# Kernel tuning notes

Measured on AMD Instinct MI355X. Metric: run time of the kernel, lower is better.

## Reference

```python
import jax, jax.numpy as jnp
import numpy as np

B, T, D, H = 4, 2048, 2048, 16
DH = D // H

def setup_inputs() -> dict:
    key = jax.random.key(0)
    ks = jax.random.split(key, 9)
    s = 1.0 / np.sqrt(D)
    return {
        "x": jax.random.normal(ks[0], (B, T, D), dtype=jnp.float32),
        "Wq": jax.random.uniform(ks[1], (D, D), jnp.float32, -s, s),
        "bq": jax.random.uniform(ks[2], (D,), jnp.float32, -s, s),
        "Wk": jax.random.uniform(ks[3], (D, D), jnp.float32, -s, s),
        "bk": jax.random.uniform(ks[4], (D,), jnp.float32, -s, s),
        "Wv": jax.random.uniform(ks[5], (D, D), jnp.float32, -s, s),
        "bv": jax.random.uniform(ks[6], (D,), jnp.float32, -s, s),
        "Wo": jax.random.uniform(ks[7], (D, D), jnp.float32, -s, s),
        "bo": jax.random.uniform(ks[8], (D,), jnp.float32, -s, s),
    }

def reference(x, Wq, bq, Wk, bk, Wv, bv, Wo, bo):
    # projections: [B,T,D] -> [B,H,T,DH]
    def split_heads(y):
        return y.reshape(B, T, H, DH).transpose(0, 2, 1, 3)
    q = split_heads(x @ Wq + bq)
    k = split_heads(x @ Wk + bk)
    v = split_heads(x @ Wv + bv)
    scale = DH ** -0.5
    scores = jnp.einsum('bhtd,bhsd->bhts', q, k) * scale  # [B,H,T,T]
    causal = jnp.tril(jnp.ones((T, T), dtype=bool))
    scores = jnp.where(causal[None, None], scores, -jnp.inf)
    weights = jax.nn.softmax(scores, axis=-1)
    out = jnp.einsum('bhts,bhsd->bhtd', weights, v)  # [B,H,T,DH]
    out = out.transpose(0, 2, 1, 3).reshape(B, T, D)
    return out @ Wo + bo
```

## Files before the change

### kernel.cpp

```cpp
#include <hip/hip_runtime.h>
#include <hip/hip_bf16.h>

#define B_  4
#define T_  2048
#define D_  2048
#define H_  16
#define DH_ 128

typedef __attribute__((ext_vector_type(4))) float f32x4;
typedef __attribute__((ext_vector_type(8))) short short8;
typedef __attribute__((ext_vector_type(4))) _Float16 half4;

__device__ __forceinline__ ushort f2bf(float f) {
    unsigned int u = __builtin_bit_cast(unsigned int, f);
    u += 0x7fffu + ((u >> 16) & 1u);
    return (ushort)(u >> 16);
}
__device__ __forceinline__ ushort f2h(float f) {
    return (ushort)(__builtin_bit_cast(unsigned int, __builtin_amdgcn_cvt_pkrtz(f, f)) & 0xffffu);
}

__device__ __forceinline__ void glds16(const void* g, void* l) {
    __builtin_amdgcn_global_load_lds(
        (const __attribute__((address_space(1))) unsigned int*)g,
        (__attribute__((address_space(3))) unsigned int*)l, 16, 0, 0);
}

__global__ void cast_f32_bf16(const float* __restrict__ x, ushort* __restrict__ xb, int n) {
    int i = (blockIdx.x * 256 + threadIdx.x) * 4;
    if (i < n) {
        float4 v = *(const float4*)(x + i);
        ushort4 o;
        o.x = f2bf(v.x); o.y = f2bf(v.y); o.z = f2bf(v.z); o.w = f2bf(v.w);
        *(ushort4*)(xb + i) = o;
    }
}

__global__ void transpose_cast(const float* __restrict__ W, ushort* __restrict__ Wt) {
    __shared__ float tile[32][33];
    int tx = threadIdx.x, ty = threadIdx.y;
    int n0 = blockIdx.x * 32, k0 = blockIdx.y * 32;
#pragma unroll
    for (int i = 0; i < 4; i++)
        tile[ty + i * 8][tx] = W[(size_t)(k0 + ty + i * 8) * D_ + n0 + tx];
    __syncthreads();
#pragma unroll
    for (int i = 0; i < 4; i++)
        Wt[(size_t)(n0 + ty + i * 8) * D_ + k0 + tx] = f2bf(tile[tx][ty + i * 8]);
}

template <int MODE>
__global__ __launch_bounds__(256, 2) void gemm_bt(
    const ushort* __restrict__ A, const ushort* __restrict__ Bt,
    const float* __restrict__ bias, void* __restrict__ Cout,
    int M, int N, int K, float oscale)
{
    extern __shared__ char smem[];
    uint4* sA = (uint4*)smem;
    uint4* sB = (uint4*)(smem + 8192);

    const int tid  = threadIdx.x;
    const int row0 = blockIdx.y * 128, col0 = blockIdx.x * 128;

    const int mA = tid >> 2, g = tid & 3;
    const int gc = g ^ ((mA >> 2) & 3);
    const ushort* pa0 = A  + (size_t)(row0 + mA) * K + gc * 8;
    const ushort* pb0 = Bt + (size_t)(col0 + mA) * K + gc * 8;

    const int lane = tid & 63, w = tid >> 6;
    const int l15 = lane & 15, quad = lane >> 4;
    const int wm = w & 1, wn = w >> 1;
    const int csel = quad ^ ((l15 >> 2) & 3);
    int aoff[4], boff[4];
#pragma unroll
    for (int mt = 0; mt < 4; mt++) aoff[mt] = (wm * 64 + mt * 16 + l15) * 4 + csel;
#pragma unroll
    for (int nt = 0; nt < 4; nt++) boff[nt] = (wn * 64 + nt * 16 + l15) * 4 + csel;

    f32x4 acc[4][4] = {};

    const int kIter = K >> 5;
    for (int kt = 0; kt < kIter; ++kt) {
        if (kt) __syncthreads();
        glds16(pa0 + kt * 32,                     sA + tid);
        glds16(pa0 + kt * 32 + (size_t)64 * K,    sA + tid + 256);
        glds16(pb0 + kt * 32,                     sB + tid);
        glds16(pb0 + kt * 32 + (size_t)64 * K,    sB + tid + 256);
        __syncthreads();
        short8 af[4], bfr[4];
#pragma unroll
        for (int mt = 0; mt < 4; mt++) af[mt]  = __builtin_bit_cast(short8, sA[aoff[mt]]);
#pragma unroll
        for (int nt = 0; nt < 4; nt++) bfr[nt] = __builtin_bit_cast(short8, sB[boff[nt]]);
#pragma unroll
        for (int mt = 0; mt < 4; mt++)
#pragma unroll
            for (int nt = 0; nt < 4; nt++)
                acc[mt][nt] = __builtin_amdgcn_mfma_f32_16x16x32_bf16(af[mt], bfr[nt], acc[mt][nt], 0, 0, 0);
    }

    if constexpr (MODE == 0 || MODE == 1) {
#pragma unroll
        for (int nt = 0; nt < 4; nt++) {
            int col = col0 + wn * 64 + nt * 16 + l15;
            float bb = bias[col];
#pragma unroll
            for (int mt = 0; mt < 4; mt++) {
                int rowb = row0 + wm * 64 + mt * 16 + quad * 4;
#pragma unroll
                for (int r = 0; r < 4; r++) {
                    float v = (acc[mt][nt][r] + bb) * oscale;
                    if constexpr (MODE == 0)
                        ((ushort*)Cout)[(size_t)(rowb + r) * N + col] = f2bf(v);
                    else
                        ((float*)Cout)[(size_t)(rowb + r) * N + col] = v;
                }
            }
        }
    } else {
        __syncthreads();
        ushort* tr = (ushort*)smem;
#pragma unroll
        for (int nt = 0; nt < 4; nt++) {
            int cl = wn * 64 + nt * 16 + l15;
            float bb = bias[col0 + cl];
#pragma unroll
            for (int mt = 0; mt < 4; mt++) {
                int rl = wm * 64 + mt * 16 + quad * 4;
#pragma unroll
                for (int r = 0; r < 4; r++)
                    tr[cl * 136 + rl + r] = f2h(acc[mt][nt][r] + bb);
            }
        }
        __syncthreads();
        ushort* C = (ushort*)Cout;
        int b = row0 >> 11, t0 = row0 & (T_ - 1), h = col0 >> 7;
        for (int idx = tid; idx < 2048; idx += 256) {
            int dh = idx >> 4, c = idx & 15;
            uint4 v = *(const uint4*)(tr + dh * 136 + c * 8);
            *(uint4*)(C + (size_t)((b * H_ + h) * DH_ + dh) * T_ + t0 + c * 8) = v;
        }
    }
}

__global__ __launch_bounds__(256, 4) void attn_kernel(
    const ushort* __restrict__ Q, const ushort* __restrict__ K,
    const ushort* __restrict__ Vt, ushort* __restrict__ O)
{
    __shared__ __align__(16) char smem[32768];
    uint4* kS = (uint4*)smem;
    uint4* vS = (uint4*)(smem + 16384);

    const int tid = threadIdx.x;
    const int bid = blockIdx.x;
    const int slot = bid >> 3;
    const int g = (bid & 7) + 8 * (slot >> 4);
    const int qx = slot & 15;
    const int b = g >> 4, h = g & 15;

    const int lane = tid & 63, w = tid >> 6, l15 = lane & 15, quad = lane >> 4;

    const int krow = tid >> 4;
    const int kchunk = (tid & 15) ^ (krow & 7);
    const ushort* kg = K + ((size_t)(b * T_) + krow) * D_ + h * DH_ + kchunk * 8;
    const int vrow = tid >> 3;
    const int vchunk = (tid & 7) ^ (vrow & 7);
    const ushort* vg = Vt + ((size_t)((b * H_ + h) * DH_) + vrow) * T_ + vchunk * 8;

    const int qts[2] = { qx, 31 - qx };

    for (int e = 0; e < 2; ++e) {
        const int qt = qts[e], q0 = qt * 64;
        const int qbase = q0 + w * 16;

        short8 aq[4];
        {
            const ushort* qp = Q + ((size_t)(b * T_) + qbase + l15) * D_ + h * DH_ + quad * 8;
#pragma unroll
            for (int ks = 0; ks < 4; ++ks)
                aq[ks] = __builtin_bit_cast(short8, *(const uint4*)(qp + ks * 32));
        }

        f32x4 accO[8] = {};
        float mrow = -INFINITY, lrow = 0.f;

        for (int it = 0; it <= qt; ++it) {
            const int s0 = it * 64;
            const int stMax = (it == qt) ? (w + 1) : 4;
            __syncthreads();
            const ushort* kp = kg + (size_t)s0 * D_;
            const ushort* vp = vg + s0;
#pragma unroll
            for (int j = 0; j < 4; ++j) glds16(kp + (size_t)j * 16 * D_, kS + j * 256 + tid);
#pragma unroll
            for (int j = 0; j < 4; ++j) glds16(vp + (size_t)j * 32 * T_, vS + j * 256 + tid);
            __syncthreads();

            f32x4 sT[4] = {};
#pragma unroll
            for (int ks = 0; ks < 4; ++ks)
#pragma unroll
                for (int st = 0; st < 4; ++st)
                    if (st < stMax) {
                        int row = st * 16 + l15;
                        short8 ak = __builtin_bit_cast(short8, kS[row * 16 + ((ks * 4 + quad) ^ (row & 7))]);
                        sT[st] = __builtin_amdgcn_mfma_f32_16x16x32_bf16(ak, aq[ks], sT[st], 0, 0, 0);
                    }

            if (s0 + 64 > qbase) {
                const int q = qbase + l15;
#pragma unroll
                for (int st = 0; st < 4; ++st)
                    if (st < stMax)
#pragma unroll
                        for (int r = 0; r < 4; ++r)
                            if (s0 + st * 16 + quad * 4 + r > q) sT[st][r] = -INFINITY;
            }

            float rmax = -INFINITY;
#pragma unroll
            for (int st = 0; st < 4; ++st)
                if (st < stMax)
#pragma unroll
                    for (int r = 0; r < 4; ++r) rmax = fmaxf(rmax, sT[st][r]);
            rmax = fmaxf(rmax, __shfl_xor(rmax, 16));
            rmax = fmaxf(rmax, __shfl_xor(rmax, 32));
            float mnew  = fmaxf(mrow, rmax);
            float alpha = __builtin_amdgcn_exp2f(mrow - mnew);
            mrow = mnew;

            float psum = 0.f;
            half4 pb[4];
#pragma unroll
            for (int st = 0; st < 4; ++st)
                if (st < stMax) {
                    float p0 = __builtin_amdgcn_exp2f(sT[st][0] - mnew);
                    float p1 = __builtin_amdgcn_exp2f(sT[st][1] - mnew);
                    float p2 = __builtin_amdgcn_exp2f(sT[st][2] - mnew);
                    float p3 = __builtin_amdgcn_exp2f(sT[st][3] - mnew);
                    psum += (p0 + p1) + (p2 + p3);
                    uint2 u;
                    u.x = __builtin_bit_cast(unsigned int, __builtin_amdgcn_cvt_pkrtz(p0, p1));
                    u.y = __builtin_bit_cast(unsigned int, __builtin_amdgcn_cvt_pkrtz(p2, p3));
                    pb[st] = __builtin_bit_cast(half4, u);
                }
            psum += __shfl_xor(psum, 16);
            psum += __shfl_xor(psum, 32);
            lrow = lrow * alpha + psum;
#pragma unroll
            for (int nt = 0; nt < 8; ++nt)
#pragma unroll
                for (int r = 0; r < 4; ++r) accO[nt][r] *= alpha;

            const ushort* vbase = (const ushort*)vS;
#pragma unroll
            for (int st = 0; st < 4; ++st)
                if (st < stMax) {
                    const int ch = (st * 2 + (quad >> 1));
                    const int sub = (quad & 1) * 4;
#pragma unroll
                    for (int nt = 0; nt < 8; ++nt) {
                        int dh = nt * 16 + l15;
                        half4 vf = *(const half4*)(vbase + dh * 64 + ((ch ^ (l15 & 7)) * 8) + sub);
                        accO[nt] = __builtin_amdgcn_mfma_f32_16x16x16f16(vf, pb[st], accO[nt], 0, 0, 0);
                    }
                }
        }

        __syncthreads();
        ushort* eT = (ushort*)smem + w * 2176;
        float inv = 1.0f / lrow;
#pragma unroll
        for (int nt = 0; nt < 8; ++nt) {
            int dh = nt * 16 + quad * 4;
#pragma unroll
            for (int r = 0; r < 4; ++r)
                eT[l15 * 136 + dh + r] = f2bf(accO[nt][r] * inv);
        }
        for (int idx = lane; idx < 256; idx += 64) {
            int row = idx >> 4, c = idx & 15;
            uint4 v = *(const uint4*)(eT + row * 136 + c * 8);
            *(uint4*)(O + ((size_t)(b * T_) + q0 + w * 16 + row) * D_ + h * DH_ + c * 8) = v;
        }
    }
}

extern "C" void kernel_launch(void* const* d_in, const int* in_sizes, int n_in,
                              void* d_out, int out_size, void* d_ws, size_t ws_size,
                              hipStream_t stream) {
    const float* x  = (const float*)d_in[0];
    const float* Wq = (const float*)d_in[1];
    const float* bq = (const float*)d_in[2];
    const float* Wk = (const float*)d_in[3];
    const float* bk = (const float*)d_in[4];
    const float* Wv = (const float*)d_in[5];
    const float* bv = (const float*)d_in[6];
    const float* Wo = (const float*)d_in[7];
    const float* bo = (const float*)d_in[8];

    char* ws = (char*)d_ws;
    const size_t MB = 1u << 20;
    ushort* xb  = (ushort*)(ws);
    ushort* Wqt = (ushort*)(ws + 32 * MB);
    ushort* Wkt = (ushort*)(ws + 40 * MB);
    ushort* Wvt = (ushort*)(ws + 48 * MB);
    ushort* Wot = (ushort*)(ws + 56 * MB);
    ushort* Qb  = (ushort*)(ws + 64 * MB);
    ushort* Kb  = (ushort*)(ws + 96 * MB);
    ushort* Vtb = (ushort*)(ws + 128 * MB);
    ushort* Ob  = (ushort*)(ws + 160 * MB);

    const int M = B_ * T_;
    const float qscale = (float)(0.08838834764831845 * 1.4426950408889634);

    cast_f32_bf16<<<(M * D_) / 1024, 256, 0, stream>>>(x, xb, M * D_);
    dim3 tb(32, 8), tg(D_ / 32, D_ / 32);
    transpose_cast<<<tg, tb, 0, stream>>>(Wq, Wqt);
    transpose_cast<<<tg, tb, 0, stream>>>(Wk, Wkt);
    transpose_cast<<<tg, tb, 0, stream>>>(Wv, Wvt);
    transpose_cast<<<tg, tb, 0, stream>>>(Wo, Wot);

    dim3 gg(D_ / 128, M / 128);
    gemm_bt<0><<<gg, 256, 16384, stream>>>(xb, Wqt, bq, Qb,  M, D_, D_, qscale);
    gemm_bt<0><<<gg, 256, 16384, stream>>>(xb, Wkt, bk, Kb,  M, D_, D_, 1.0f);
    gemm_bt<2><<<gg, 256, 34816, stream>>>(xb, Wvt, bv, Vtb, M, D_, D_, 1.0f);

    attn_kernel<<<dim3(1024), 256, 0, stream>>>(Qb, Kb, Vtb, Ob);

    gemm_bt<1><<<gg, 256, 16384, stream>>>(Ob, Wot, bo, (float*)d_out, M, D_, D_, 1.0f);
}
```

Before: 635.5 us.

## Fuse QKV projections into one launch and restructure attention V staging

```diff
diff --git a/kernel.cpp b/kernel.cpp
--- a/kernel.cpp
+++ b/kernel.cpp
@@ -49,18 +49,24 @@
         Wt[(size_t)(n0 + ty + i * 8) * D_ + k0 + tx] = f2bf(tile[tx][ty + i * 8]);
 }
 
-template <int MODE>
-__global__ __launch_bounds__(256, 2) void gemm_bt(
-    const ushort* __restrict__ A, const ushort* __restrict__ Bt,
-    const float* __restrict__ bias, void* __restrict__ Cout,
-    int M, int N, int K, float oscale)
+__global__ __launch_bounds__(256, 3) void gemm_qkv(
+    const ushort* __restrict__ A,
+    const ushort* __restrict__ Wq, const ushort* __restrict__ Wk, const ushort* __restrict__ Wv,
+    const float* __restrict__ bq, const float* __restrict__ bk, const float* __restrict__ bv,
+    ushort* __restrict__ Qb, ushort* __restrict__ Kb, ushort* __restrict__ Vtb,
+    float qscale)
 {
     extern __shared__ char smem[];
     uint4* sA = (uint4*)smem;
     uint4* sB = (uint4*)(smem + 8192);
 
     const int tid  = threadIdx.x;
-    const int row0 = blockIdx.y * 128, col0 = blockIdx.x * 128;
+    const int sel  = blockIdx.x >> 4;
+    const int row0 = blockIdx.y * 128, col0 = (blockIdx.x & 15) * 128;
+    const ushort* Bt = (sel == 0) ? Wq : (sel == 1) ? Wk : Wv;
+    const float* bias = (sel == 0) ? bq : (sel == 1) ? bk : bv;
+    const float oscale = (sel == 0) ? qscale : 1.0f;
+    const int K = D_, N = D_;
 
     const int mA = tid >> 2, g = tid & 3;
     const int gc = g ^ ((mA >> 2) & 3);
@@ -99,7 +105,8 @@
                 acc[mt][nt] = __builtin_amdgcn_mfma_f32_16x16x32_bf16(af[mt], bfr[nt], acc[mt][nt], 0, 0, 0);
     }
 
-    if constexpr (MODE == 0 || MODE == 1) {
+    if (sel < 2) {
+        ushort* Cout = (sel == 0) ? Qb : Kb;
 #pragma unroll
         for (int nt = 0; nt < 4; nt++) {
             int col = col0 + wn * 64 + nt * 16 + l15;
@@ -108,13 +115,8 @@
             for (int mt = 0; mt < 4; mt++) {
                 int rowb = row0 + wm * 64 + mt * 16 + quad * 4;
 #pragma unroll
-                for (int r = 0; r < 4; r++) {
-                    float v = (acc[mt][nt][r] + bb) * oscale;
-                    if constexpr (MODE == 0)
-                        ((ushort*)Cout)[(size_t)(rowb + r) * N + col] = f2bf(v);
-                    else
-                        ((float*)Cout)[(size_t)(rowb + r) * N + col] = v;
-                }
+                for (int r = 0; r < 4; r++)
+                    Cout[(size_t)(rowb + r) * N + col] = f2bf((acc[mt][nt][r] + bb) * oscale);
             }
         }
     } else {
@@ -133,23 +135,85 @@
             }
         }
         __syncthreads();
-        ushort* C = (ushort*)Cout;
         int b = row0 >> 11, t0 = row0 & (T_ - 1), h = col0 >> 7;
         for (int idx = tid; idx < 2048; idx += 256) {
             int dh = idx >> 4, c = idx & 15;
             uint4 v = *(const uint4*)(tr + dh * 136 + c * 8);
-            *(uint4*)(C + (size_t)((b * H_ + h) * DH_ + dh) * T_ + t0 + c * 8) = v;
-        }
-    }
-}
-
-__global__ __launch_bounds__(256, 4) void attn_kernel(
+            *(uint4*)(Vtb + (size_t)((b * H_ + h) * DH_ + dh) * T_ + t0 + c * 8) = v;
+        }
+    }
+}
+
+__global__ __launch_bounds__(256, 3) void gemm_bt_f32(
+    const ushort* __restrict__ A, const ushort* __restrict__ Bt,
+    const float* __restrict__ bias, float* __restrict__ Cout,
+    int M, int N, int K)
+{
+    extern __shared__ char smem[];
+    uint4* sA = (uint4*)smem;
+    uint4* sB = (uint4*)(smem + 8192);
+
+    const int tid  = threadIdx.x;
+    const int row0 = blockIdx.y * 128, col0 = blockIdx.x * 128;
+
+    const int mA = tid >> 2, g = tid & 3;
+    const int gc = g ^ ((mA >> 2) & 3);
+    const ushort* pa0 = A  + (size_t)(row0 + mA) * K + gc * 8;
+    const ushort* pb0 = Bt + (size_t)(col0 + mA) * K + gc * 8;
+
+    const int lane = tid & 63, w = tid >> 6;
+    const int l15 = lane & 15, quad = lane >> 4;
+    const int wm = w & 1, wn = w >> 1;
+    const int csel = quad ^ ((l15 >> 2) & 3);
+    int aoff[4], boff[4];
+#pragma unroll
+    for (int mt = 0; mt < 4; mt++) aoff[mt] = (wm * 64 + mt * 16 + l15) * 4 + csel;
+#pragma unroll
+    for (int nt = 0; nt < 4; nt++) boff[nt] = (wn * 64 + nt * 16 + l15) * 4 + csel;
+
+    f32x4 acc[4][4] = {};
+
+    const int kIter = K >> 5;
+    for (int kt = 0; kt < kIter; ++kt) {
+        if (kt) __syncthreads();
+        glds16(pa0 + kt * 32,                     sA + tid);
+        glds16(pa0 + kt * 32 + (size_t)64 * K,    sA + tid + 256);
+        glds16(pb0 + kt * 32,                     sB + tid);
+        glds16(pb0 + kt * 32 + (size_t)64 * K,    sB + tid + 256);
+        __syncthreads();
+        short8 af[4], bfr[4];
+#pragma unroll
+        for (int mt = 0; mt < 4; mt++) af[mt]  = __builtin_bit_cast(short8, sA[aoff[mt]]);
+#pragma unroll
+        for (int nt = 0; nt < 4; nt++) bfr[nt] = __builtin_bit_cast(short8, sB[boff[nt]]);
+#pragma unroll
+        for (int mt = 0; mt < 4; mt++)
+#pragma unroll
+            for (int nt = 0; nt < 4; nt++)
+                acc[mt][nt] = __builtin_amdgcn_mfma_f32_16x16x32_bf16(af[mt], bfr[nt], acc[mt][nt], 0, 0, 0);
+    }
+
+#pragma unroll
+    for (int nt = 0; nt < 4; nt++) {
+        int col = col0 + wn * 64 + nt * 16 + l15;
+        float bb = bias[col];
+#pragma unroll
+        for (int mt = 0; mt < 4; mt++) {
+            int rowb = row0 + wm * 64 + mt * 16 + quad * 4;
+#pragma unroll
+            for (int r = 0; r < 4; r++)
+                Cout[(size_t)(rowb + r) * N + col] = acc[mt][nt][r] + bb;
+        }
+    }
+}
+
+__global__ __launch_bounds__(256, 5) void attn_kernel(
     const ushort* __restrict__ Q, const ushort* __restrict__ K,
     const ushort* __restrict__ Vt, ushort* __restrict__ O)
 {
     __shared__ __align__(16) char smem[32768];
-    uint4* kS = (uint4*)smem;
-    uint4* vS = (uint4*)(smem + 16384);
+    uint4*  kS = (uint4*)smem;
+    ushort* vS = (ushort*)(smem + 16384);
 
     const int tid = threadIdx.x;
     const int bid = blockIdx.x;
@@ -163,9 +227,11 @@
     const int krow = tid >> 4;
     const int kchunk = (tid & 15) ^ (krow & 7);
     const ushort* kg = K + ((size_t)(b * T_) + krow) * D_ + h * DH_ + kchunk * 8;
-    const int vrow = tid >> 3;
-    const int vchunk = (tid & 7) ^ (vrow & 7);
-    const ushort* vg = Vt + ((size_t)((b * H_ + h) * DH_) + vrow) * T_ + vchunk * 8;
+
+    const int vrow = tid >> 3, vc = tid & 7;
+    const ushort* vg = Vt + ((size_t)((b * H_ + h) * DH_) + vrow) * T_ + vc * 8;
+    const int vs0 = ((2 * vc    ) ^ (vrow & 15)) * 4;
+    const int vs1 = ((2 * vc + 1) ^ (vrow & 15)) * 4;
 
     const int qts[2] = { qx, 31 - qx };
 
@@ -184,16 +250,21 @@
         f32x4 accO[8] = {};
         float mrow = -INFINITY, lrow = 0.f;
 
-        for (int it = 0; it <= qt; ++it) {
-            const int s0 = it * 64;
-            const int stMax = (it == qt) ? (w + 1) : 4;
+        auto tile = [&](int s0, int stMax, bool diag) {
             __syncthreads();
             const ushort* kp = kg + (size_t)s0 * D_;
+#pragma unroll
+            for (int j = 0; j < 4; ++j) glds16(kp + (size_t)j * 16 * D_, kS + j * 256 + tid);
             const ushort* vp = vg + s0;
-#pragma unroll
-            for (int j = 0; j < 4; ++j) glds16(kp + (size_t)j * 16 * D_, kS + j * 256 + tid);
-#pragma unroll
-            for (int j = 0; j < 4; ++j) glds16(vp + (size_t)j * 32 * T_, vS + j * 256 + tid);
+            uint4 vv[4];
+#pragma unroll
+            for (int j = 0; j < 4; ++j) vv[j] = *(const uint4*)(vp + (size_t)j * 32 * T_);
+#pragma unroll
+            for (int j = 0; j < 4; ++j) {
+                ushort* dst = vS + (j * 32 + vrow) * 64;
+                *(uint2*)(dst + vs0) = make_uint2(vv[j].x, vv[j].y);
+                *(uint2*)(dst + vs1) = make_uint2(vv[j].z, vv[j].w);
+            }
             __syncthreads();
 
             f32x4 sT[4] = {};
@@ -207,14 +278,12 @@
                         sT[st] = __builtin_amdgcn_mfma_f32_16x16x32_bf16(ak, aq[ks], sT[st], 0, 0, 0);
                     }
 
-            if (s0 + 64 > qbase) {
+            if (diag) {
                 const int q = qbase + l15;
-#pragma unroll
-                for (int st = 0; st < 4; ++st)
-                    if (st < stMax)
-#pragma unroll
-                        for (int r = 0; r < 4; ++r)
-                            if (s0 + st * 16 + quad * 4 + r > q) sT[st][r] = -INFINITY;
+                const int st = stMax - 1;
+#pragma unroll
+                for (int r = 0; r < 4; ++r)
+                    if (s0 + st * 16 + quad * 4 + r > q) sT[st][r] = -INFINITY;
             }
 
             float rmax = -INFINITY;
@@ -252,20 +321,20 @@
 #pragma unroll
                 for (int r = 0; r < 4; ++r) accO[nt][r] *= alpha;
 
-            const ushort* vbase = (const ushort*)vS;
 #pragma unroll
             for (int st = 0; st < 4; ++st)
                 if (st < stMax) {
-                    const int ch = (st * 2 + (quad >> 1));
-                    const int sub = (quad & 1) * 4;
 #pragma unroll
                     for (int nt = 0; nt < 8; ++nt) {
                         int dh = nt * 16 + l15;
-                        half4 vf = *(const half4*)(vbase + dh * 64 + ((ch ^ (l15 & 7)) * 8) + sub);
+                        half4 vf = *(const half4*)(vS + dh * 64 + (((st * 4 + quad) ^ l15) * 4));
                         accO[nt] = __builtin_amdgcn_mfma_f32_16x16x16f16(vf, pb[st], accO[nt], 0, 0, 0);
                     }
                 }
-        }
+        };
+
+        for (int it = 0; it < qt; ++it) tile(it * 64, 4, false);
+        tile(qt * 64, w + 1, true);
 
         __syncthreads();
         ushort* eT = (ushort*)smem + w * 2176;
@@ -320,12 +389,11 @@
     transpose_cast<<<tg, tb, 0, stream>>>(Wv, Wvt);
     transpose_cast<<<tg, tb, 0, stream>>>(Wo, Wot);
 
-    dim3 gg(D_ / 128, M / 128);
-    gemm_bt<0><<<gg, 256, 16384, stream>>>(xb, Wqt, bq, Qb,  M, D_, D_, qscale);
-    gemm_bt<0><<<gg, 256, 16384, stream>>>(xb, Wkt, bk, Kb,  M, D_, D_, 1.0f);
-    gemm_bt<2><<<gg, 256, 34816, stream>>>(xb, Wvt, bv, Vtb, M, D_, D_, 1.0f);
+    gemm_qkv<<<dim3(48, M / 128), 256, 34816, stream>>>(
+        xb, Wqt, Wkt, Wvt, bq, bk, bv, Qb, Kb, Vtb, qscale);
 
     attn_kernel<<<dim3(1024), 256, 0, stream>>>(Qb, Kb, Vtb, Ob);
 
-    gemm_bt<1><<<gg, 256, 16384, stream>>>(Ob, Wot, bo, (float*)d_out, M, D_, D_, 1.0f);
-}
+    gemm_bt_f32<<<dim3(D_ / 128, M / 128), 256, 16384, stream>>>(
+        Ob, Wot, bo, (float*)d_out, M, D_, D_);
+}
```

New measurement: 616.7 us. -3.0%, faster.
